# Optimization experiments

Hardware: AMD Instinct MI355X
Metric: run time of the kernel (lower is better)

The kernel has to match this reference:

```python
import jax, jax.numpy as jnp
import numpy as np

N = 100000        # nodes
E = 1600000       # edges (avg degree 16)
F = 128           # num_features
H = 8             # heads
D = F // H        # head_dim


def setup_inputs() -> dict:
    key = jax.random.key(0)
    ks = jax.random.split(key, 11)
    s = 1.0 / np.sqrt(F)
    return {
        "feat": jax.random.normal(ks[0], (N, F), dtype=jnp.float32),
        "edge_src": jax.random.randint(ks[1], (E,), 0, N, dtype=jnp.int32),
        "edge_dst": jax.random.randint(ks[2], (E,), 0, N, dtype=jnp.int32),
        "Wq": jax.random.uniform(ks[3], (F, F), jnp.float32, -s, s),
        "bq": jax.random.uniform(ks[4], (F,), jnp.float32, -s, s),
        "Wk": jax.random.uniform(ks[5], (F, F), jnp.float32, -s, s),
        "bk": jax.random.uniform(ks[6], (F,), jnp.float32, -s, s),
        "Wv": jax.random.uniform(ks[7], (F, F), jnp.float32, -s, s),
        "bv": jax.random.uniform(ks[8], (F,), jnp.float32, -s, s),
        "Wo": jax.random.uniform(ks[9], (F, F), jnp.float32, -s, s),
        "bo": jax.random.uniform(ks[10], (F,), jnp.float32, -s, s),
    }


def reference(feat, edge_src, edge_dst, Wq, bq, Wk, bk, Wv, bv, Wo, bo):
    scale = D ** -0.5
    # projections, split into heads: [N, H, D]
    q = ((feat @ Wq.T + bq) * scale).reshape(N, H, D)
    k = (feat @ Wk.T + bk).reshape(N, H, D)
    v = (feat @ Wv.T + bv).reshape(N, H, D)

    # per-edge dot product k[src] . q[dst] -> [E, H]  (dfn.u_dot_v)
    scores = jnp.einsum('ehd,ehd->eh', k[edge_src], q[edge_dst])

    # edge softmax normalized over incoming edges of each dst node
    m = jax.ops.segment_max(scores, edge_dst, num_segments=N)  # [N, H]
    m = jnp.where(jnp.isfinite(m), m, 0.0)
    e = jnp.exp(scores - m[edge_dst])                          # [E, H]
    z = jax.ops.segment_sum(e, edge_dst, num_segments=N)       # [N, H]
    alpha = e / z[edge_dst]                                    # [E, H]

    # weighted sum aggregation (u_mul_e + sum): [N, H, D]
    wv = alpha[:, :, None] * v[edge_src]                       # [E, H, D]
    attn = jax.ops.segment_sum(wv, edge_dst, num_segments=N)

    return attn.reshape(N, F) @ Wo.T + bo
```

## Files before the change

### kernel.cpp

```cpp
#include <hip/hip_runtime.h>
#include <math.h>

#define N_NODES 100000
#define N_EDGES 1600000
#define FDIM 128
#define NHEAD 8
#define HDIM 16
#define SCAT_PHASES 4

using bf16x8 = __attribute__((ext_vector_type(8))) short;
using half8  = __attribute__((ext_vector_type(8))) _Float16;
using half2t = __attribute__((ext_vector_type(2))) _Float16;
using f32x4  = __attribute__((ext_vector_type(4))) float;
using f32x2  = __attribute__((ext_vector_type(2))) float;

__device__ inline unsigned short f2bf(float f) {
    union { float f; unsigned int u; } x; x.f = f;
    unsigned int u = x.u;
    return (unsigned short)((u + 0x7fffu + ((u >> 16) & 1u)) >> 16);
}
__device__ inline unsigned short f2h(float f) {
    _Float16 h = (_Float16)f;
    return __builtin_bit_cast(unsigned short, h);
}
__device__ inline unsigned int packh2(float a, float b) {
    return (unsigned int)f2h(a) | ((unsigned int)f2h(b) << 16);
}
__device__ inline float h_lo(unsigned int u) {
    return (float)__builtin_bit_cast(_Float16, (unsigned short)(u & 0xffffu));
}
__device__ inline float h_hi(unsigned int u) {
    return (float)__builtin_bit_cast(_Float16, (unsigned short)(u >> 16));
}
__device__ inline float exp2_fast(float x) {
#if __has_builtin(__builtin_amdgcn_exp2f)
    return __builtin_amdgcn_exp2f(x);
#else
    return __expf(x * 0.6931471805599453f);
#endif
}

#if __has_builtin(__builtin_amdgcn_cvt_pk_fp8_f32)
__device__ inline unsigned char fp8_enc(float x) {
    return (unsigned char)(__builtin_amdgcn_cvt_pk_fp8_f32(x, x, 0, false) & 0xff);
}
#else
__device__ inline unsigned char fp8_enc(float x) {
    unsigned int u = __builtin_bit_cast(unsigned int, x);
    unsigned int s = (u >> 24) & 0x80;
    float ax = fabsf(x);
    if (!(ax >= 0.001953125f)) {
        int m = (int)(ax * 512.f + 0.5f);
        return (unsigned char)(s | (unsigned)(m > 7 ? 7 : m));
    }
    if (ax > 448.f) return (unsigned char)(s | 0x7e);
    int e; float fr = frexpf(ax, &e);
    int q = (int)(fr * 16.f + 0.5f);
    if (q == 16) { q = 8; e += 1; }
    int exp = e - 1 + 7;
    if (exp <= 0) { int m = (int)(ax * 512.f + 0.5f); return (unsigned char)(s | (unsigned)(m > 7 ? 7 : m)); }
    if (exp > 15) return (unsigned char)(s | 0x7e);
    return (unsigned char)(s | (exp << 3) | (q & 7));
}
#endif

#if __has_builtin(__builtin_amdgcn_cvt_pk_f32_fp8)
#define FP8_HW_DECODE 1
#else
__device__ inline float fp8_dec_sw(unsigned char b) {
    int s = b >> 7, e = (b >> 3) & 15, m = b & 7;
    float v = (e == 0) ? ldexpf((float)m, -9) : ldexpf((float)(8 + m), e - 10);
    return s ? -v : v;
}
#endif

__device__ inline float dot_fp8_16(uint4 kr, const f32x2* __restrict__ qq2) {
#ifdef FP8_HW_DECODE
    f32x2 a = {0.f, 0.f};
    f32x2 p;
    p = __builtin_amdgcn_cvt_pk_f32_fp8(kr.x, false); a += p * qq2[0];
    p = __builtin_amdgcn_cvt_pk_f32_fp8(kr.x, true);  a += p * qq2[1];
    p = __builtin_amdgcn_cvt_pk_f32_fp8(kr.y, false); a += p * qq2[2];
    p = __builtin_amdgcn_cvt_pk_f32_fp8(kr.y, true);  a += p * qq2[3];
    p = __builtin_amdgcn_cvt_pk_f32_fp8(kr.z, false); a += p * qq2[4];
    p = __builtin_amdgcn_cvt_pk_f32_fp8(kr.z, true);  a += p * qq2[5];
    p = __builtin_amdgcn_cvt_pk_f32_fp8(kr.w, false); a += p * qq2[6];
    p = __builtin_amdgcn_cvt_pk_f32_fp8(kr.w, true);  a += p * qq2[7];
    return a[0] + a[1];
#else
    const float* qq = (const float*)qq2;
    float s = 0.f;
    unsigned int wds[4] = {kr.x, kr.y, kr.z, kr.w};
#pragma unroll
    for (int i = 0; i < 4; ++i)
#pragma unroll
        for (int j = 0; j < 4; ++j)
            s = fmaf(fp8_dec_sw((wds[i] >> (8 * j)) & 0xff), qq[i * 4 + j], s);
    return s;
#endif
}

__global__ __launch_bounds__(256) void convert_w_kernel(
    const float* __restrict__ W0, const float* __restrict__ W1,
    const float* __restrict__ W2, const float* __restrict__ W3,
    unsigned short* __restrict__ out)
{
    int i = blockIdx.x * 256 + threadIdx.x;
    int j  = i & 7;
    int l  = (i >> 3) & 63;
    int fk = i >> 9;
    int ks = fk & 3, nf = fk >> 2;
    int s = (nf * 16 + (l & 15)) * FDIM + ks * 32 + (l >> 4) * 8 + j;
    out[i]             = f2bf(W0[s]);
    out[16384 + i]     = f2bf(W1[s]);
    out[2 * 16384 + i] = f2bf(W2[s]);
    out[3 * 16384 + i] = f2h(W3[s]);
}

struct GemmArgs {
    const unsigned short* W[3];
    const float* b[3];
    void* out[3];
    float scale[3];
};

template<int NP, bool IN_F32, bool MFMA_F16, int OUTM>
__global__ __launch_bounds__(256, 2) void mfma_gemm_v2(
    const void* __restrict__ Ain, GemmArgs ga, int nrows)
{
    __shared__ unsigned short A_s[128][136];
    __shared__ unsigned short W_sh[8192];

    const int t  = threadIdx.x;
    const int r0 = blockIdx.x * 128;

#pragma unroll
    for (int it = 0; it < 8; ++it) {
        int i = t + it * 256;
        int r = i >> 4, c8 = (i & 15) << 3;
        int gr = r0 + r;
        if (IN_F32) {
            float4 v0 = make_float4(0.f, 0.f, 0.f, 0.f), v1 = v0;
            if (gr < nrows) {
                const float* Af = (const float*)Ain;
                v0 = *(const float4*)&Af[(size_t)gr * FDIM + c8];
                v1 = *(const float4*)&Af[(size_t)gr * FDIM + c8 + 4];
            }
            uint4 pk;
            pk.x = (unsigned)f2bf(v0.x) | ((unsigned)f2bf(v0.y) << 16);
            pk.y = (unsigned)f2bf(v0.z) | ((unsigned)f2bf(v0.w) << 16);
            pk.z = (unsigned)f2bf(v1.x) | ((unsigned)f2bf(v1.y) << 16);
            pk.w = (unsigned)f2bf(v1.z) | ((unsigned)f2bf(v1.w) << 16);
            *(uint4*)&A_s[r][c8] = pk;
        } else {
            uint4 v = make_uint4(0u, 0u, 0u, 0u);
            if (gr < nrows) {
                const unsigned short* Ab = (const unsigned short*)Ain;
                v = *(const uint4*)&Ab[(size_t)gr * FDIM + c8];
            }
            *(uint4*)&A_s[r][c8] = v;
        }
    }
    __syncthreads();

    const int w  = t >> 6, l = t & 63;
    const int lr = l & 15, lk = l >> 4;

    bf16x8 a[2][4];
#pragma unroll
    for (int rg = 0; rg < 2; ++rg)
#pragma unroll
        for (int ks = 0; ks < 4; ++ks)
            a[rg][ks] = *(const bf16x8*)&A_s[w * 32 + rg * 16 + lr][ks * 32 + lk * 8];

#pragma unroll
    for (int p = 0; p < NP; ++p) {
        const unsigned short* Wsrc = ga.W[p];
        f32x4 acc[2][8];
#pragma unroll
        for (int rg = 0; rg < 2; ++rg)
#pragma unroll
            for (int nf = 0; nf < 8; ++nf) acc[rg][nf] = (f32x4){0.f, 0.f, 0.f, 0.f};

#pragma unroll
        for (int h = 0; h < 2; ++h) {
#pragma unroll
            for (int it = 0; it < 4; ++it) {
                int chunk = t + it * 256;
                *(uint4*)&W_sh[chunk * 8] = *(const uint4*)&Wsrc[h * 8192 + chunk * 8];
            }
            __syncthreads();
#pragma unroll
            for (int nfl = 0; nfl < 4; ++nfl) {
                int nf = h * 4 + nfl;
#pragma unroll
                for (int ks = 0; ks < 4; ++ks) {
                    bf16x8 bfr = *(const bf16x8*)&W_sh[((nfl * 4 + ks) * 64 + l) * 8];
                    if (MFMA_F16) {
                        acc[0][nf] = __builtin_amdgcn_mfma_f32_16x16x32_f16(
                            __builtin_bit_cast(half8, a[0][ks]), __builtin_bit_cast(half8, bfr),
                            acc[0][nf], 0, 0, 0);
                        acc[1][nf] = __builtin_amdgcn_mfma_f32_16x16x32_f16(
                            __builtin_bit_cast(half8, a[1][ks]), __builtin_bit_cast(half8, bfr),
                            acc[1][nf], 0, 0, 0);
                    } else {
                        acc[0][nf] = __builtin_amdgcn_mfma_f32_16x16x32_bf16(a[0][ks], bfr, acc[0][nf], 0, 0, 0);
                        acc[1][nf] = __builtin_amdgcn_mfma_f32_16x16x32_bf16(a[1][ks], bfr, acc[1][nf], 0, 0, 0);
                    }
                }
            }
            __syncthreads();
        }

        const float* bias = ga.b[p];
        const float  scl  = ga.scale[p];
        const int    mode = (OUTM >> (2 * p)) & 3;

        if (mode == 0) {
            unsigned short* Oh = &A_s[0][0];
#pragma unroll
            for (int rg = 0; rg < 2; ++rg)
#pragma unroll
                for (int nf = 0; nf < 8; ++nf) {
                    int col = nf * 16 + lr;
                    float bv = bias[col];
#pragma unroll
                    for (int j = 0; j < 4; ++j)
                        Oh[(w * 32 + rg * 16 + lk * 4 + j) * 136 + col] = f2h((acc[rg][nf][j] + bv) * scl);
                }
            __syncthreads();
            unsigned short* outp = (unsigned short*)ga.out[p];
#pragma unroll
            for (int it = 0; it < 8; ++it) {
                int i = t + it * 256;
                int r = i >> 4, c8 = (i & 15) << 3;
                if (r0 + r < nrows)
                    *(uint4*)&outp[(size_t)(r0 + r) * FDIM + c8] = *(const uint4*)&Oh[r * 136 + c8];
            }
        } else if (mode == 1) {
            unsigned char* O8 = (unsigned char*)A_s;
#pragma unroll
            for (int rg = 0; rg < 2; ++rg)
#pragma unroll
                for (int nf = 0; nf < 8; ++nf) {
                    int col = nf * 16 + lr;
                    float bv = bias[col];
#pragma unroll
                    for (int j = 0; j < 4; ++j)
                        O8[(w * 32 + rg * 16 + lk * 4 + j) * 144 + col] = fp8_enc((acc[rg][nf][j] + bv) * scl);
                }
            __syncthreads();
            unsigned char* outp = (unsigned char*)ga.out[p];
#pragma unroll
            for (int it = 0; it < 4; ++it) {
                int i = t + it * 256;
                int r = i >> 3, c16 = (i & 7) << 4;
                if (r0 + r < nrows)
                    *(uint4*)&outp[(size_t)(r0 + r) * FDIM + c16] = *(const uint4*)&O8[r * 144 + c16];
            }
        } else {
            float* outp = (float*)ga.out[p];
#pragma unroll
            for (int rg = 0; rg < 2; ++rg)
#pragma unroll
                for (int nf = 0; nf < 8; ++nf) {
                    int col = nf * 16 + lr;
                    float bv = bias[col];
                    int row = r0 + w * 32 + rg * 16 + lk * 4;
#pragma unroll
                    for (int j = 0; j < 4; ++j)
                        if (row + j < nrows)
                            outp[(size_t)(row + j) * FDIM + col] = (acc[rg][nf][j] + bv) * scl;
                }
        }
    }
}

__global__ void count_rank_kernel(const int* __restrict__ dst, int* __restrict__ cnt,
                                  unsigned short* __restrict__ rank, int n)
{
    int i = blockIdx.x * 256 + threadIdx.x;
    if (i < n) {
        int d = __builtin_nontemporal_load(&dst[i]);
        rank[i] = (unsigned short)atomicAdd(&cnt[d], 1);
    }
}

__global__ void scan_a_kernel(const int* __restrict__ cnt, int* __restrict__ row_off,
                              int* __restrict__ part, int n)
{
    __shared__ int s[256];
    int t = threadIdx.x;
    int gid = blockIdx.x * 256 + t;
    int x = (gid < n) ? cnt[gid] : 0;
    s[t] = x;
    __syncthreads();
    for (int off = 1; off < 256; off <<= 1) {
        int val = (t >= off) ? s[t - off] : 0;
        __syncthreads();
        s[t] += val;
        __syncthreads();
    }
    if (gid < n) row_off[gid] = s[t] - x;
    if (t == 255) part[blockIdx.x] = s[255];
}

__global__ void scan_b_kernel(int* __restrict__ part, int nb)
{
    __shared__ int s[512];
    int t = threadIdx.x;
    int x = (t < nb) ? part[t] : 0;
    s[t] = x;
    __syncthreads();
    for (int off = 1; off < 512; off <<= 1) {
        int val = (t >= off) ? s[t - off] : 0;
        __syncthreads();
        s[t] += val;
        __syncthreads();
    }
    if (t < nb) part[t] = s[t] - x;
}

__global__ void scan_c_kernel(int* __restrict__ row_off, const int* __restrict__ part,
                              int n, int total)
{
    int gid = blockIdx.x * 256 + threadIdx.x;
    if (gid < n) row_off[gid] += part[blockIdx.x];
    if (gid == 0) row_off[n] = total;
}

__global__ void scatter_phase_kernel(const int* __restrict__ src, const int* __restrict__ dst,
                                     const unsigned short* __restrict__ rank,
                                     const int* __restrict__ row_off,
                                     int* __restrict__ csr_src, int n, int lo, int hi)
{
    int i = blockIdx.x * 256 + threadIdx.x;
    if (i < n) {
        int d = __builtin_nontemporal_load(&dst[i]);
        if (d >= lo && d < hi) {
            int pos = row_off[d] + (int)__builtin_nontemporal_load(&rank[i]);
            csr_src[pos] = __builtin_nontemporal_load(&src[i]);
        }
    }
}

__global__ __launch_bounds__(256) void attn_kernel(
    const unsigned short* __restrict__ q, const unsigned char* __restrict__ kf8,
    const unsigned short* __restrict__ v,
    const int* __restrict__ row_off, const int* __restrict__ csr_src,
    unsigned short* __restrict__ out, int nnodes)
{
    __shared__ float q_s[4][NHEAD][18];
    __shared__ float p_s[4][64][NHEAD];
    __shared__ int   src_s[4][64];

    const int w = threadIdx.x >> 6;
    const int l = threadIdx.x & 63;
    const int node = blockIdx.x * 4 + w;
    if (node >= nnodes) return;

    {
        unsigned int qv = *(const unsigned int*)&q[(size_t)node * FDIM + l * 2];
        *(f32x2*)&q_s[w][l >> 3][(l & 7) * 2] = (f32x2){h_lo(qv), h_hi(qv)};
    }

    const int e_l = l >> 3, h_sc = l & 7;
    const int e2 = l >> 4, h_ag = (l >> 1) & 7, dq = l & 1;
    const int vo = h_ag * HDIM + dq * 8;

    const int start = row_off[node];
    const int end   = row_off[node + 1];

    float z_run = 0.f;
    f32x2 acc[4] = {{0.f,0.f},{0.f,0.f},{0.f,0.f},{0.f,0.f}};

    const f32x2* qq2 = (const f32x2*)&q_s[w][h_sc][0];

    for (int c0 = start; c0 < end; c0 += 64) {
        const int cn = min(64, end - c0);

        for (int i = l; i < cn; i += 64)
            src_s[w][i] = csr_src[c0 + i];

        for (int base = 0; base < cn; base += 32) {
            uint4 kr[4];
#pragma unroll
            for (int it = 0; it < 4; ++it) {
                int ei = base + it * 8 + e_l;
                if (ei < cn)
                    kr[it] = *(const uint4*)&kf8[(size_t)src_s[w][ei] * FDIM + h_sc * 16];
            }
#pragma unroll
            for (int it = 0; it < 4; ++it) {
                int ei = base + it * 8 + e_l;
                if (ei < cn) {
                    float p = exp2_fast(dot_fp8_16(kr[it], qq2));
                    p_s[w][ei][h_sc] = p;
                    z_run += p;
                }
            }
        }

        for (int base = 0; base < cn; base += 4) {
            int e  = base + e2;
            int ec = min(e, cn - 1);
            float p = (e < cn) ? p_s[w][e][h_ag] : 0.f;
            uint4 vv = *(const uint4*)&v[(size_t)src_s[w][ec] * FDIM + vo];
            f32x2 p2 = {p, p};
            acc[0] += p2 * (f32x2){h_lo(vv.x), h_hi(vv.x)};
            acc[1] += p2 * (f32x2){h_lo(vv.y), h_hi(vv.y)};
            acc[2] += p2 * (f32x2){h_lo(vv.z), h_hi(vv.z)};
            acc[3] += p2 * (f32x2){h_lo(vv.w), h_hi(vv.w)};
        }
    }

#pragma unroll
    for (int mask = 8; mask < 64; mask <<= 1)
        z_run += __shfl_xor(z_run, mask, 64);

#pragma unroll
    for (int mask = 16; mask < 64; mask <<= 1)
#pragma unroll
        for (int i = 0; i < 4; ++i) {
            acc[i][0] += __shfl_xor(acc[i][0], mask, 64);
            acc[i][1] += __shfl_xor(acc[i][1], mask, 64);
        }

    float z_ag = __shfl(z_run, h_ag, 64);

    if (e2 == 0) {
        uint4 o = make_uint4(0u, 0u, 0u, 0u);
        if (end > start) {
            float rz = 1.0f / z_ag;
            o.x = packh2(acc[0][0] * rz, acc[0][1] * rz);
            o.y = packh2(acc[1][0] * rz, acc[1][1] * rz);
            o.z = packh2(acc[2][0] * rz, acc[2][1] * rz);
            o.w = packh2(acc[3][0] * rz, acc[3][1] * rz);
        }
        *(uint4*)&out[(size_t)node * FDIM + vo] = o;
    }
}

extern "C" void kernel_launch(void* const* d_in, const int* in_sizes, int n_in,
                              void* d_out, int out_size, void* d_ws, size_t ws_size,
                              hipStream_t stream)
{
    const float* feat = (const float*)d_in[0];
    const int*   esrc = (const int*)d_in[1];
    const int*   edst = (const int*)d_in[2];
    const float* Wq   = (const float*)d_in[3];
    const float* bq   = (const float*)d_in[4];
    const float* Wk   = (const float*)d_in[5];
    const float* bk   = (const float*)d_in[6];
    const float* Wv   = (const float*)d_in[7];
    const float* bv   = (const float*)d_in[8];
    const float* Wo   = (const float*)d_in[9];
    const float* bo   = (const float*)d_in[10];
    float* out = (float*)d_out;

    const size_t NROW = (size_t)N_NODES * FDIM;
    unsigned short* qb  = (unsigned short*)d_ws;
    unsigned short* vb  = qb + NROW;
    unsigned short* ab  = vb + NROW;
    unsigned char*  kf8 = (unsigned char*)(ab + NROW);
    unsigned short* wbf = (unsigned short*)(kf8 + NROW);
    unsigned short* rank = wbf + 4 * 16384;
    int* cnt     = (int*)(rank + N_EDGES);
    int* row_off = cnt + N_NODES;
    int* part    = row_off + N_NODES + 1;
    int* csr_src = part + 512;

    const int gemmGrid = (N_NODES + 127) / 128;
    const int edgeGrid = (N_EDGES + 255) / 256;
    const int nb       = (N_NODES + 255) / 256;

    hipLaunchKernelGGL(convert_w_kernel, dim3(64), dim3(256), 0, stream,
                       Wq, Wk, Wv, Wo, wbf);

    GemmArgs qkv;
    qkv.W[0] = wbf;          qkv.b[0] = bq; qkv.out[0] = qb;  qkv.scale[0] = 0.25f * 1.4426950408889634f;
    qkv.W[1] = wbf + 16384;  qkv.b[1] = bk; qkv.out[1] = kf8; qkv.scale[1] = 1.0f;
    qkv.W[2] = wbf + 32768;  qkv.b[2] = bv; qkv.out[2] = vb;  qkv.scale[2] = 1.0f;
    hipLaunchKernelGGL((mfma_gemm_v2<3, true, false, 4>), dim3(gemmGrid), dim3(256), 0, stream,
                       feat, qkv, N_NODES);

    hipMemsetAsync(cnt, 0, sizeof(int) * N_NODES, stream);
    hipLaunchKernelGGL(count_rank_kernel, dim3(edgeGrid), dim3(256), 0, stream,
                       edst, cnt, rank, N_EDGES);
    hipLaunchKernelGGL(scan_a_kernel, dim3(nb), dim3(256), 0, stream, cnt, row_off, part, N_NODES);
    hipLaunchKernelGGL(scan_b_kernel, dim3(1), dim3(512), 0, stream, part, nb);
    hipLaunchKernelGGL(scan_c_kernel, dim3(nb), dim3(256), 0, stream, row_off, part, N_NODES, N_EDGES);
    for (int ph = 0; ph < SCAT_PHASES; ++ph) {
        int lo = (int)((long long)N_NODES * ph / SCAT_PHASES);
        int hi = (int)((long long)N_NODES * (ph + 1) / SCAT_PHASES);
        hipLaunchKernelGGL(scatter_phase_kernel, dim3(edgeGrid), dim3(256), 0, stream,
                           esrc, edst, rank, row_off, csr_src, N_EDGES, lo, hi);
    }

    hipLaunchKernelGGL(attn_kernel, dim3((N_NODES + 3) / 4), dim3(256), 0, stream,
                       qb, kf8, vb, row_off, csr_src, ab, N_NODES);

    GemmArgs oprj;
    oprj.W[0] = wbf + 3 * 16384; oprj.b[0] = bo; oprj.out[0] = out; oprj.scale[0] = 1.0f;
    hipLaunchKernelGGL((mfma_gemm_v2<1, false, true, 2>), dim3(gemmGrid), dim3(256), 0, stream,
                       ab, oprj, N_NODES);
}
```

Baseline: 276.2 us.

## Fuse edge counting into QKV GEMM launch and merge scan/scatter kernels

```diff
diff --git a/kernel.cpp b/kernel.cpp
--- a/kernel.cpp
+++ b/kernel.cpp
@@ -7,10 +7,10 @@
 #define NHEAD 8
 #define HDIM 16
 #define SCAT_PHASES 4
+#define COUNT_BLOCKS 2048
 
 using bf16x8 = __attribute__((ext_vector_type(8))) short;
 using half8  = __attribute__((ext_vector_type(8))) _Float16;
-using half2t = __attribute__((ext_vector_type(2))) _Float16;
 using f32x4  = __attribute__((ext_vector_type(4))) float;
 using f32x2  = __attribute__((ext_vector_type(2))) float;
 
@@ -103,7 +103,7 @@
 __global__ __launch_bounds__(256) void convert_w_kernel(
     const float* __restrict__ W0, const float* __restrict__ W1,
     const float* __restrict__ W2, const float* __restrict__ W3,
-    unsigned short* __restrict__ out)
+    unsigned short* __restrict__ out, int* __restrict__ cnt)
 {
     int i = blockIdx.x * 256 + threadIdx.x;
     int j  = i & 7;
@@ -115,6 +115,8 @@
     out[16384 + i]     = f2bf(W1[s]);
     out[2 * 16384 + i] = f2bf(W2[s]);
     out[3 * 16384 + i] = f2h(W3[s]);
+    for (int c = i; c < N_NODES; c += 64 * 256)
+        cnt[c] = 0;
 }
 
 struct GemmArgs {
@@ -125,14 +127,14 @@
 };
 
 template<int NP, bool IN_F32, bool MFMA_F16, int OUTM>
-__global__ __launch_bounds__(256, 2) void mfma_gemm_v2(
-    const void* __restrict__ Ain, GemmArgs ga, int nrows)
+__device__ __forceinline__ void gemm_body(const void* __restrict__ Ain,
+                                          const GemmArgs& ga, int nrows, int blk)
 {
     __shared__ unsigned short A_s[128][136];
     __shared__ unsigned short W_sh[8192];
 
     const int t  = threadIdx.x;
-    const int r0 = blockIdx.x * 128;
+    const int r0 = blk * 128;
 
 #pragma unroll
     for (int it = 0; it < 8; ++it) {
@@ -276,13 +278,30 @@
     }
 }
 
-__global__ void count_rank_kernel(const int* __restrict__ dst, int* __restrict__ cnt,
-                                  unsigned short* __restrict__ rank, int n)
-{
-    int i = blockIdx.x * 256 + threadIdx.x;
-    if (i < n) {
-        int d = __builtin_nontemporal_load(&dst[i]);
-        rank[i] = (unsigned short)atomicAdd(&cnt[d], 1);
+template<int NP, bool IN_F32, bool MFMA_F16, int OUTM>
+__global__ __launch_bounds__(256, 2) void mfma_gemm_v2(
+    const void* __restrict__ Ain, GemmArgs ga, int nrows)
+{
+    gemm_body<NP, IN_F32, MFMA_F16, OUTM>(Ain, ga, nrows, blockIdx.x);
+}
+
+template<int NP, bool IN_F32, bool MFMA_F16, int OUTM>
+__global__ __launch_bounds__(256, 2) void gemm_count_kernel(
+    const void* __restrict__ Ain, GemmArgs ga, int nrows, int nGemmBlocks,
+    const int* __restrict__ edst, int* __restrict__ cnt,
+    unsigned int* __restrict__ pk, int nEdges)
+{
+    const int b = blockIdx.x;
+    if (b < nGemmBlocks) {
+        gemm_body<NP, IN_F32, MFMA_F16, OUTM>(Ain, ga, nrows, b);
+        return;
+    }
+    int i = (b - nGemmBlocks) * 256 + threadIdx.x;
+    const int stride = COUNT_BLOCKS * 256;
+    for (; i < nEdges; i += stride) {
+        int d = __builtin_nontemporal_load(&edst[i]);
+        unsigned r = (unsigned)atomicAdd(&cnt[d], 1);
+        pk[i] = ((unsigned)d << 8) | (r & 0xffu);
     }
 }
 
@@ -321,34 +340,31 @@
     if (t < nb) part[t] = s[t] - x;
 }
 
-__global__ void scan_c_kernel(int* __restrict__ row_off, const int* __restrict__ part,
-                              int n, int total)
-{
-    int gid = blockIdx.x * 256 + threadIdx.x;
-    if (gid < n) row_off[gid] += part[blockIdx.x];
-    if (gid == 0) row_off[n] = total;
-}
-
-__global__ void scatter_phase_kernel(const int* __restrict__ src, const int* __restrict__ dst,
-                                     const unsigned short* __restrict__ rank,
-                                     const int* __restrict__ row_off,
-                                     int* __restrict__ csr_src, int n, int lo, int hi)
-{
-    int i = blockIdx.x * 256 + threadIdx.x;
-    if (i < n) {
-        int d = __builtin_nontemporal_load(&dst[i]);
-        if (d >= lo && d < hi) {
-            int pos = row_off[d] + (int)__builtin_nontemporal_load(&rank[i]);
-            csr_src[pos] = __builtin_nontemporal_load(&src[i]);
-        }
+__global__ void scatter_all_kernel(const int* __restrict__ src,
+                                   const unsigned int* __restrict__ pk,
+                                   const int* __restrict__ row_off,
+                                   const int* __restrict__ part,
+                                   int* __restrict__ csr_src, int n, int blocksPerPhase)
+{
+    int phase = blockIdx.x / blocksPerPhase;
+    int i = (blockIdx.x % blocksPerPhase) * 256 + threadIdx.x;
+    if (i >= n) return;
+    int lo = (int)((long long)N_NODES * phase / SCAT_PHASES);
+    int hi = (int)((long long)N_NODES * (phase + 1) / SCAT_PHASES);
+    unsigned p = __builtin_nontemporal_load(&pk[i]);
+    int d = (int)(p >> 8);
+    if (d >= lo && d < hi) {
+        int pos = row_off[d] + part[d >> 8] + (int)(p & 0xffu);
+        csr_src[pos] = __builtin_nontemporal_load(&src[i]);
     }
 }
 
 __global__ __launch_bounds__(256) void attn_kernel(
     const unsigned short* __restrict__ q, const unsigned char* __restrict__ kf8,
     const unsigned short* __restrict__ v,
-    const int* __restrict__ row_off, const int* __restrict__ csr_src,
-    unsigned short* __restrict__ out, int nnodes)
+    const int* __restrict__ row_off, const int* __restrict__ part,
+    const int* __restrict__ csr_src,
+    unsigned short* __restrict__ out, int nnodes, int nedges)
 {
     __shared__ float q_s[4][NHEAD][18];
     __shared__ float p_s[4][64][NHEAD];
@@ -368,8 +384,9 @@
     const int e2 = l >> 4, h_ag = (l >> 1) & 7, dq = l & 1;
     const int vo = h_ag * HDIM + dq * 8;
 
-    const int start = row_off[node];
-    const int end   = row_off[node + 1];
+    const int start = row_off[node] + part[node >> 8];
+    const int end   = (node == nnodes - 1) ? nedges
+                      : row_off[node + 1] + part[(node + 1) >> 8];
 
     float z_run = 0.f;
     f32x2 acc[4] = {{0.f,0.f},{0.f,0.f},{0.f,0.f},{0.f,0.f}};
@@ -464,8 +481,8 @@
     unsigned short* ab  = vb + NROW;
     unsigned char*  kf8 = (unsigned char*)(ab + NROW);
     unsigned short* wbf = (unsigned short*)(kf8 + NROW);
-    unsigned short* rank = wbf + 4 * 16384;
-    int* cnt     = (int*)(rank + N_EDGES);
+    unsigned int* pk = (unsigned int*)(wbf + 4 * 16384);
+    int* cnt     = (int*)(pk + N_EDGES);
     int* row_off = cnt + N_NODES;
     int* part    = row_off + N_NODES + 1;
     int* csr_src = part + 512;
@@ -475,30 +492,24 @@
     const int nb       = (N_NODES + 255) / 256;
 
     hipLaunchKernelGGL(convert_w_kernel, dim3(64), dim3(256), 0, stream,
-                       Wq, Wk, Wv, Wo, wbf);
+                       Wq, Wk, Wv, Wo, wbf, cnt);
 
     GemmArgs qkv;
     qkv.W[0] = wbf;          qkv.b[0] = bq; qkv.out[0] = qb;  qkv.scale[0] = 0.25f * 1.4426950408889634f;
     qkv.W[1] = wbf + 16384;  qkv.b[1] = bk; qkv.out[1] = kf8; qkv.scale[1] = 1.0f;
     qkv.W[2] = wbf + 32768;  qkv.b[2] = bv; qkv.out[2] = vb;  qkv.scale[2] = 1.0f;
-    hipLaunchKernelGGL((mfma_gemm_v2<3, true, false, 4>), dim3(gemmGrid), dim3(256), 0, stream,
-                       feat, qkv, N_NODES);
-
-    hipMemsetAsync(cnt, 0, sizeof(int) * N_NODES, stream);
-    hipLaunchKernelGGL(count_rank_kernel, dim3(edgeGrid), dim3(256), 0, stream,
-                       edst, cnt, rank, N_EDGES);
+    hipLaunchKernelGGL((gemm_count_kernel<3, true, false, 4>),
+                       dim3(gemmGrid + COUNT_BLOCKS), dim3(256), 0, stream,
+                       feat, qkv, N_NODES, gemmGrid, edst, cnt, pk, N_EDGES);
+
     hipLaunchKernelGGL(scan_a_kernel, dim3(nb), dim3(256), 0, stream, cnt, row_off, part, N_NODES);
     hipLaunchKernelGGL(scan_b_kernel, dim3(1), dim3(512), 0, stream, part, nb);
-    hipLaunchKernelGGL(scan_c_kernel, dim3(nb), dim3(256), 0, stream, row_off, part, N_NODES, N_EDGES);
-    for (int ph = 0; ph < SCAT_PHASES; ++ph) {
-        int lo = (int)((long long)N_NODES * ph / SCAT_PHASES);
-        int hi = (int)((long long)N_NODES * (ph + 1) / SCAT_PHASES);
-        hipLaunchKernelGGL(scatter_phase_kernel, dim3(edgeGrid), dim3(256), 0, stream,
-                           esrc, edst, rank, row_off, csr_src, N_EDGES, lo, hi);
-    }
+
+    hipLaunchKernelGGL(scatter_all_kernel, dim3(edgeGrid * SCAT_PHASES), dim3(256), 0, stream,
+                       esrc, pk, row_off, part, csr_src, N_EDGES, edgeGrid);
 
     hipLaunchKernelGGL(attn_kernel, dim3((N_NODES + 3) / 4), dim3(256), 0, stream,
-                       qb, kf8, vb, row_off, csr_src, ab, N_NODES);
+                       qb, kf8, vb, row_off, part, csr_src, ab, N_NODES, N_EDGES);
 
     GemmArgs oprj;
     oprj.W[0] = wbf + 3 * 16384; oprj.b[0] = bo; oprj.out[0] = out; oprj.scale[0] = 1.0f;
```

After: 288.9 us. 4.6% more time.

## Build CSR with two-level bucketed radix partition instead of global atomics

Applied to the files above, without the earlier changes.

```diff
diff --git a/kernel.cpp b/kernel.cpp
--- a/kernel.cpp
+++ b/kernel.cpp
@@ -6,11 +6,12 @@
 #define FDIM 128
 #define NHEAD 8
 #define HDIM 16
-#define SCAT_PHASES 4
+#define NBUK 391
+#define NPART 400
+#define PCHUNK 4000
 
 using bf16x8 = __attribute__((ext_vector_type(8))) short;
 using half8  = __attribute__((ext_vector_type(8))) _Float16;
-using half2t = __attribute__((ext_vector_type(2))) _Float16;
 using f32x4  = __attribute__((ext_vector_type(4))) float;
 using f32x2  = __attribute__((ext_vector_type(2))) float;
 
@@ -117,6 +118,115 @@
     out[3 * 16384 + i] = f2h(W3[s]);
 }
 
+__global__ __launch_bounds__(256) void csr_hist_kernel(
+    const int* __restrict__ edst, int* __restrict__ cntmatT)
+{
+    __shared__ int hist[NBUK];
+    for (int b = threadIdx.x; b < NBUK; b += 256) hist[b] = 0;
+    __syncthreads();
+    const int c0 = blockIdx.x * PCHUNK;
+    const int ce = min(c0 + PCHUNK, N_EDGES);
+    for (int i = c0 + threadIdx.x; i < ce; i += 256) {
+        int d = __builtin_nontemporal_load(&edst[i]);
+        atomicAdd(&hist[d >> 8], 1);
+    }
+    __syncthreads();
+    for (int b = threadIdx.x; b < NBUK; b += 256)
+        cntmatT[b * NPART + blockIdx.x] = hist[b];
+}
+
+__global__ __launch_bounds__(512) void csr_colscan_kernel(
+    const int* __restrict__ cntmatT, int* __restrict__ preT, int* __restrict__ colsum)
+{
+    __shared__ int s[512];
+    const int t = threadIdx.x, buk = blockIdx.x;
+    int x = (t < NPART) ? cntmatT[buk * NPART + t] : 0;
+    s[t] = x;
+    __syncthreads();
+    for (int off = 1; off < 512; off <<= 1) {
+        int v = (t >= off) ? s[t - off] : 0;
+        __syncthreads();
+        s[t] += v;
+        __syncthreads();
+    }
+    if (t < NPART) preT[buk * NPART + t] = s[t] - x;
+    if (t == NPART - 1) colsum[buk] = s[t];
+}
+
+__global__ __launch_bounds__(512) void csr_basescan_kernel(
+    const int* __restrict__ colsum, int* __restrict__ base, int* __restrict__ row_off)
+{
+    __shared__ int s[512];
+    const int t = threadIdx.x;
+    int x = (t < NBUK) ? colsum[t] : 0;
+    s[t] = x;
+    __syncthreads();
+    for (int off = 1; off < 512; off <<= 1) {
+        int v = (t >= off) ? s[t - off] : 0;
+        __syncthreads();
+        s[t] += v;
+        __syncthreads();
+    }
+    if (t < NBUK) base[t] = s[t] - x;
+    if (t == 0) { base[NBUK] = N_EDGES; row_off[N_NODES] = N_EDGES; }
+}
+
+__global__ __launch_bounds__(256) void csr_partition_kernel(
+    const int* __restrict__ esrc, const int* __restrict__ edst,
+    const int* __restrict__ preT, const int* __restrict__ base,
+    uint2* __restrict__ bpair)
+{
+    __shared__ int cur[NBUK];
+    for (int b = threadIdx.x; b < NBUK; b += 256)
+        cur[b] = base[b] + preT[b * NPART + blockIdx.x];
+    __syncthreads();
+    const int c0 = blockIdx.x * PCHUNK;
+    const int ce = min(c0 + PCHUNK, N_EDGES);
+    for (int i = c0 + threadIdx.x; i < ce; i += 256) {
+        int d = __builtin_nontemporal_load(&edst[i]);
+        int s = __builtin_nontemporal_load(&esrc[i]);
+        int slot = atomicAdd(&cur[d >> 8], 1);
+        bpair[slot] = make_uint2((unsigned)s, (unsigned)d);
+    }
+}
+
+__global__ __launch_bounds__(256) void csr_bucket_kernel(
+    const uint2* __restrict__ bpair, const int* __restrict__ base,
+    int* __restrict__ row_off, int* __restrict__ csr_src)
+{
+    __shared__ int cnt2[256], s[256], cur[256];
+    const int buk = blockIdx.x, t = threadIdx.x;
+    const int b0 = base[buk];
+    const int sz = base[buk + 1] - b0;
+    const int nb0 = buk << 8;
+
+    cnt2[t] = 0;
+    __syncthreads();
+    for (int i = t; i < sz; i += 256)
+        atomicAdd(&cnt2[bpair[b0 + i].y & 255u], 1);
+    __syncthreads();
+
+    int x = cnt2[t];
+    s[t] = x;
+    __syncthreads();
+    for (int off = 1; off < 256; off <<= 1) {
+        int v = (t >= off) ? s[t - off] : 0;
+        __syncthreads();
+        s[t] += v;
+        __syncthreads();
+    }
+    int excl = s[t] - x;
+    cur[t] = excl;
+    if (nb0 + t < N_NODES) row_off[nb0 + t] = b0 + excl;
+    __syncthreads();
+
+    for (int i = t; i < sz; i += 256) {
+        uint2 p = bpair[b0 + i];
+        int r = atomicAdd(&cur[p.y & 255u], 1);
+        csr_src[b0 + r] = (int)p.x;
+    }
+}
+
 struct GemmArgs {
     const unsigned short* W[3];
     const float* b[3];
@@ -276,74 +386,6 @@
     }
 }
 
-__global__ void count_rank_kernel(const int* __restrict__ dst, int* __restrict__ cnt,
-                                  unsigned short* __restrict__ rank, int n)
-{
-    int i = blockIdx.x * 256 + threadIdx.x;
-    if (i < n) {
-        int d = __builtin_nontemporal_load(&dst[i]);
-        rank[i] = (unsigned short)atomicAdd(&cnt[d], 1);
-    }
-}
-
-__global__ void scan_a_kernel(const int* __restrict__ cnt, int* __restrict__ row_off,
-                              int* __restrict__ part, int n)
-{
-    __shared__ int s[256];
-    int t = threadIdx.x;
-    int gid = blockIdx.x * 256 + t;
-    int x = (gid < n) ? cnt[gid] : 0;
-    s[t] = x;
-    __syncthreads();
-    for (int off = 1; off < 256; off <<= 1) {
-        int val = (t >= off) ? s[t - off] : 0;
-        __syncthreads();
-        s[t] += val;
-        __syncthreads();
-    }
-    if (gid < n) row_off[gid] = s[t] - x;
-    if (t == 255) part[blockIdx.x] = s[255];
-}
-
-__global__ void scan_b_kernel(int* __restrict__ part, int nb)
-{
-    __shared__ int s[512];
-    int t = threadIdx.x;
-    int x = (t < nb) ? part[t] : 0;
-    s[t] = x;
-    __syncthreads();
-    for (int off = 1; off < 512; off <<= 1) {
-        int val = (t >= off) ? s[t - off] : 0;
-        __syncthreads();
-        s[t] += val;
-        __syncthreads();
-    }
-    if (t < nb) part[t] = s[t] - x;
-}
-
-__global__ void scan_c_kernel(int* __restrict__ row_off, const int* __restrict__ part,
-                              int n, int total)
-{
-    int gid = blockIdx.x * 256 + threadIdx.x;
-    if (gid < n) row_off[gid] += part[blockIdx.x];
-    if (gid == 0) row_off[n] = total;
-}
-
-__global__ void scatter_phase_kernel(const int* __restrict__ src, const int* __restrict__ dst,
-                                     const unsigned short* __restrict__ rank,
-                                     const int* __restrict__ row_off,
-                                     int* __restrict__ csr_src, int n, int lo, int hi)
-{
-    int i = blockIdx.x * 256 + threadIdx.x;
-    if (i < n) {
-        int d = __builtin_nontemporal_load(&dst[i]);
-        if (d >= lo && d < hi) {
-            int pos = row_off[d] + (int)__builtin_nontemporal_load(&rank[i]);
-            csr_src[pos] = __builtin_nontemporal_load(&src[i]);
-        }
-    }
-}
-
 __global__ __launch_bounds__(256) void attn_kernel(
     const unsigned short* __restrict__ q, const unsigned char* __restrict__ kf8,
     const unsigned short* __restrict__ v,
@@ -464,15 +506,15 @@
     unsigned short* ab  = vb + NROW;
     unsigned char*  kf8 = (unsigned char*)(ab + NROW);
     unsigned short* wbf = (unsigned short*)(kf8 + NROW);
-    unsigned short* rank = wbf + 4 * 16384;
-    int* cnt     = (int*)(rank + N_EDGES);
-    int* row_off = cnt + N_NODES;
-    int* part    = row_off + N_NODES + 1;
-    int* csr_src = part + 512;
+    int* cntmatT = (int*)(wbf + 4 * 16384);
+    int* preT    = cntmatT + NBUK * NPART;
+    int* colsum  = preT + NBUK * NPART;
+    int* base    = colsum + 512;
+    uint2* bpair = (uint2*)(base + 512);
+    int* row_off = (int*)(bpair + N_EDGES);
+    int* csr_src = row_off + N_NODES + 1;
 
     const int gemmGrid = (N_NODES + 127) / 128;
-    const int edgeGrid = (N_EDGES + 255) / 256;
-    const int nb       = (N_NODES + 255) / 256;
 
     hipLaunchKernelGGL(convert_w_kernel, dim3(64), dim3(256), 0, stream,
                        Wq, Wk, Wv, Wo, wbf);
@@ -484,18 +526,13 @@
     hipLaunchKernelGGL((mfma_gemm_v2<3, true, false, 4>), dim3(gemmGrid), dim3(256), 0, stream,
                        feat, qkv, N_NODES);
 
-    hipMemsetAsync(cnt, 0, sizeof(int) * N_NODES, stream);
-    hipLaunchKernelGGL(count_rank_kernel, dim3(edgeGrid), dim3(256), 0, stream,
-                       edst, cnt, rank, N_EDGES);
-    hipLaunchKernelGGL(scan_a_kernel, dim3(nb), dim3(256), 0, stream, cnt, row_off, part, N_NODES);
-    hipLaunchKernelGGL(scan_b_kernel, dim3(1), dim3(512), 0, stream, part, nb);
-    hipLaunchKernelGGL(scan_c_kernel, dim3(nb), dim3(256), 0, stream, row_off, part, N_NODES, N_EDGES);
-    for (int ph = 0; ph < SCAT_PHASES; ++ph) {
-        int lo = (int)((long long)N_NODES * ph / SCAT_PHASES);
-        int hi = (int)((long long)N_NODES * (ph + 1) / SCAT_PHASES);
-        hipLaunchKernelGGL(scatter_phase_kernel, dim3(edgeGrid), dim3(256), 0, stream,
-                           esrc, edst, rank, row_off, csr_src, N_EDGES, lo, hi);
-    }
+    hipLaunchKernelGGL(csr_hist_kernel, dim3(NPART), dim3(256), 0, stream, edst, cntmatT);
+    hipLaunchKernelGGL(csr_colscan_kernel, dim3(NBUK), dim3(512), 0, stream, cntmatT, preT, colsum);
+    hipLaunchKernelGGL(csr_basescan_kernel, dim3(1), dim3(512), 0, stream, colsum, base, row_off);
+    hipLaunchKernelGGL(csr_partition_kernel, dim3(NPART), dim3(256), 0, stream,
+                       esrc, edst, preT, base, bpair);
+    hipLaunchKernelGGL(csr_bucket_kernel, dim3(NBUK), dim3(256), 0, stream,
+                       bpair, base, row_off, csr_src);
 
     hipLaunchKernelGGL(attn_kernel, dim3((N_NODES + 3) / 4), dim3(256), 0, stream,
                        qb, kf8, vb, row_off, csr_src, ab, N_NODES);
```

Result: faster. 222.7 us, median of 2 (-19.4%).
